# Optimization experiments

Measured on AMD Instinct MI355X. Metric: run time of the kernel, lower is better.

Reference implementation:

```python
import jax, jax.numpy as jnp
import numpy as np

T, B, X, Y = 24, 16, 64, 64
S, M, C = 16, 8, 8
F = S + M + C   # GRU input_size = 32
H = 32          # hidden_size


def setup_inputs() -> dict:
    key = jax.random.key(0)
    ks = jax.random.split(key, 8)
    inv = 1.0 / np.sqrt(H)
    return {
        "spatial": jax.random.normal(ks[0], (T, B, X, Y, S), dtype=jnp.float32),
        "meteorology": jax.random.normal(ks[1], (T, B, X, Y, M), dtype=jnp.float32),
        "context": jax.random.normal(ks[2], (T, B, X, Y, C), dtype=jnp.float32),
        # GRU parameters (torch layout: [3H, F] and [3H, H], gate order r,z,n)
        "W_ih": jax.random.uniform(ks[3], (3 * H, F), jnp.float32, -inv, inv),
        "W_hh": jax.random.uniform(ks[4], (3 * H, H), jnp.float32, -inv, inv),
        "b_ih": jax.random.uniform(ks[5], (3 * H,), jnp.float32, -inv, inv),
        "b_hh": jax.random.uniform(ks[6], (3 * H,), jnp.float32, -inv, inv),
        # output projection (hidden -> spatial_size)
        "W": jax.random.normal(ks[7], (H, S), dtype=jnp.float32),
    }


def reference(spatial, meteorology, context, W_ih, W_hh, b_ih, b_hh, W):
    # cat features: (T, B, X, Y, F); merge all pixels + batch into one GRU batch
    x = jnp.concatenate((spatial, meteorology, context), axis=4)
    N = B * X * Y
    x = x.reshape(T, N, F)

    # precompute input projections for all timesteps: (T, N, 3H)
    gx_all = jnp.einsum('tnf,gf->tng', x, W_ih) + b_ih

    def step(h, gx):
        gh = h @ W_hh.T + b_hh                      # (N, 3H)
        r = jax.nn.sigmoid(gx[:, :H] + gh[:, :H])
        z = jax.nn.sigmoid(gx[:, H:2 * H] + gh[:, H:2 * H])
        n = jnp.tanh(gx[:, 2 * H:] + r * gh[:, 2 * H:])
        h = (1.0 - z) * n + z * h
        return h, None

    h0 = jnp.zeros((N, H), dtype=x.dtype)
    h_final, _ = jax.lax.scan(step, h0, gx_all)     # (N, H)

    out = h_final @ W                               # (N, S)
    return out.reshape(B, X, Y, S)
```

## Files before the change

### kernel.cpp

```cpp
#include <hip/hip_runtime.h>
#include <hip/hip_bf16.h>


#define TSTEPS 24
#define NPIX 65536
#define PADW 40

typedef __attribute__((ext_vector_type(8))) short bf16x8;
typedef __attribute__((ext_vector_type(4))) float f32x4;
typedef __attribute__((ext_vector_type(4))) unsigned int u32x4;

#define MFMA16(a, b, c) __builtin_amdgcn_mfma_f32_16x16x32_bf16((a), (b), (c), 0, 0, 0)

#define SCL_RZ (-1.4426950408889634f)
#define SCL_N  ( 2.8853900817779268f)

__device__ __forceinline__ unsigned short f2bf(float f) {
  unsigned u = __builtin_bit_cast(unsigned, f);
  u += 0x7fffu + ((u >> 16) & 1u);
  return (unsigned short)(u >> 16);
}

__device__ __forceinline__ unsigned pk2(float a, float b) {
  __hip_bfloat162 h = __float22bfloat162_rn(float2{a, b});
  unsigned u;
  __builtin_memcpy(&u, &h, sizeof(u));
  return u;
}

__device__ __forceinline__ bf16x8 pack8(f32x4 a, f32x4 b) {
  u32x4 r = { pk2(a[0], a[1]), pk2(a[2], a[3]), pk2(b[0], b[1]), pk2(b[2], b[3]) };
  return __builtin_bit_cast(bf16x8, r);
}

__device__ __forceinline__ float sig2(float t) {
  return __builtin_amdgcn_rcpf(1.f + __builtin_amdgcn_exp2f(t));
}
__device__ __forceinline__ float tanh2(float t) {
  return 1.f - 2.f * __builtin_amdgcn_rcpf(1.f + __builtin_amdgcn_exp2f(t));
}

__device__ __forceinline__ bf16x8 relayout_h(const f32x4 h0, const f32x4 h1, int lane) {
  unsigned p00 = pk2(h0[0], h0[1]), p01 = pk2(h0[2], h0[3]);
  unsigned p10 = pk2(h1[0], h1[1]), p11 = pk2(h1[2], h1[3]);
  const int lo = (lane & 15) | ((lane & 16) << 1);
  const int hi = lo + 16;
  unsigned a0 = (unsigned)__shfl((int)p00, lo, 64);
  unsigned a1 = (unsigned)__shfl((int)p01, lo, 64);
  unsigned a2 = (unsigned)__shfl((int)p00, hi, 64);
  unsigned a3 = (unsigned)__shfl((int)p01, hi, 64);
  unsigned b0 = (unsigned)__shfl((int)p10, lo, 64);
  unsigned b1 = (unsigned)__shfl((int)p11, lo, 64);
  unsigned b2 = (unsigned)__shfl((int)p10, hi, 64);
  unsigned b3 = (unsigned)__shfl((int)p11, hi, 64);
  const bool t1 = (lane & 32) != 0;
  u32x4 d = { t1 ? b0 : a0, t1 ? b1 : a1, t1 ? b2 : a2, t1 ? b3 : a3 };
  return __builtin_bit_cast(bf16x8, d);
}

__global__ __launch_bounds__(256, 3)
void gru_fused(const float* __restrict__ spatial, const float* __restrict__ met,
               const float* __restrict__ ctx,
               const float* __restrict__ W_ih, const float* __restrict__ W_hh,
               const float* __restrict__ b_ih, const float* __restrict__ b_hh,
               const float* __restrict__ Wout, float* __restrict__ out) {
  __shared__ __align__(16) unsigned short sW[192 * PADW];
  __shared__ __align__(16) float sCB[64];
  __shared__ __align__(16) float sBIN[32];
  __shared__ __align__(16) float sBHN[32];

  const int tid = threadIdx.x;
  for (int i = tid; i < 96 * 32; i += 256) {
    int r = i >> 5, c = i & 31;
    float s = (r < 64) ? SCL_RZ : SCL_N;
    sW[r * PADW + c] = f2bf(W_ih[i] * s);
    sW[(96 + r) * PADW + c] = f2bf(W_hh[i] * s);
  }
  if (tid < 64) sCB[tid] = (b_ih[tid] + b_hh[tid]) * SCL_RZ;
  else if (tid < 96) sBIN[tid - 64] = b_ih[tid] * SCL_N;
  else if (tid < 128) sBHN[tid - 96] = b_hh[tid - 32] * SCL_N;
  __syncthreads();

  const int lane = tid & 63;
  const int col = lane & 15;
  const int q = lane >> 4;
  const int wave = blockIdx.x * 4 + (tid >> 6);
  const long p0 = (long)wave * 16 + col;

  f32x4 cS[4];
#pragma unroll
  for (int i = 0; i < 4; ++i) cS[i] = *(const f32x4*)&sCB[i * 16 + q * 4];
  const f32x4 cG4 = *(const f32x4*)&sBIN[q * 4];
  const f32x4 cG5 = *(const f32x4*)&sBIN[16 + q * 4];
  const f32x4 cH4 = *(const f32x4*)&sBHN[q * 4];
  const f32x4 cH5 = *(const f32x4*)&sBHN[16 + q * 4];

  const int wb = col * PADW + q * 8;
  const bf16x8 a0 = *(const bf16x8*)&sW[wb];
  const bf16x8 a1 = *(const bf16x8*)&sW[wb + 16 * PADW];
  const bf16x8 a2 = *(const bf16x8*)&sW[wb + 32 * PADW];
  const bf16x8 a3 = *(const bf16x8*)&sW[wb + 48 * PADW];
  const bf16x8 a4 = *(const bf16x8*)&sW[wb + 64 * PADW];
  const bf16x8 a5 = *(const bf16x8*)&sW[wb + 80 * PADW];
  const bf16x8 w0 = *(const bf16x8*)&sW[wb + 96 * PADW];
  const bf16x8 w1 = *(const bf16x8*)&sW[wb + 112 * PADW];
  const bf16x8 w2 = *(const bf16x8*)&sW[wb + 128 * PADW];
  const bf16x8 w3 = *(const bf16x8*)&sW[wb + 144 * PADW];
  const bf16x8 w4 = *(const bf16x8*)&sW[wb + 160 * PADW];
  const bf16x8 w5 = *(const bf16x8*)&sW[wb + 176 * PADW];

  const float* xp0;
  long xstride;
  if (q < 2) {
    xp0 = spatial + p0 * 16 + q * 8;
    xstride = (long)NPIX * 16;
  } else if (q == 2) {
    xp0 = met + p0 * 8; xstride = (long)NPIX * 8;
  } else {
    xp0 = ctx + p0 * 8; xstride = (long)NPIX * 8;
  }

  bf16x8 bx = pack8(*(const f32x4*)xp0, *(const f32x4*)(xp0 + 4));
  xp0 += xstride;

  f32x4 h0a = {0.f, 0.f, 0.f, 0.f}, h0b = {0.f, 0.f, 0.f, 0.f};
  const f32x4 zero = {0.f, 0.f, 0.f, 0.f};

#pragma unroll 1
  for (int t = 0; t < TSTEPS; ++t) {
    f32x4 xna, xnb;
    if (t < TSTEPS - 1) {
      xna = *(const f32x4*)xp0; xnb = *(const f32x4*)(xp0 + 4);
      xp0 += xstride;
    }

    f32x4 g0 = MFMA16(a0, bx, cS[0]);
    f32x4 g1 = MFMA16(a1, bx, cS[1]);
    f32x4 g2 = MFMA16(a2, bx, cS[2]);
    f32x4 g3 = MFMA16(a3, bx, cS[3]);
    f32x4 g4 = MFMA16(a4, bx, cG4);
    f32x4 g5 = MFMA16(a5, bx, cG5);

    bf16x8 bh = relayout_h(h0a, h0b, lane);

    f32x4 r0 = MFMA16(w0, bh, g0);
    f32x4 r1 = MFMA16(w1, bh, g1);
    f32x4 z0 = MFMA16(w2, bh, g2);
    f32x4 z1 = MFMA16(w3, bh, g3);
    f32x4 h4 = MFMA16(w4, bh, cH4);
    f32x4 h5 = MFMA16(w5, bh, cH5);

#pragma unroll
    for (int r = 0; r < 4; ++r) {
      float ra = sig2(r0[r]);
      float rb = sig2(r1[r]);
      float za = sig2(z0[r]);
      float zb = sig2(z1[r]);
      float na = tanh2(__builtin_fmaf(ra, h4[r], g4[r]));
      float nb = tanh2(__builtin_fmaf(rb, h5[r], g5[r]));
      h0a[r] = na + za * (h0a[r] - na);
      h0b[r] = nb + zb * (h0b[r] - nb);
    }

    if (t < TSTEPS - 1) bx = pack8(xna, xnb);
  }

  bf16x8 bhf = relayout_h(h0a, h0b, lane);
  float w[8];
#pragma unroll
  for (int j = 0; j < 8; ++j) w[j] = Wout[(q * 8 + j) * 16 + col];
  u32x4 awp = { pk2(w[0], w[1]), pk2(w[2], w[3]), pk2(w[4], w[5]), pk2(w[6], w[7]) };
  bf16x8 aw = __builtin_bit_cast(bf16x8, awp);
  f32x4 o0 = MFMA16(aw, bhf, zero);
  *(f32x4*)&out[p0 * 16 + q * 4] = o0;
}

extern "C" void kernel_launch(void* const* d_in, const int* in_sizes, int n_in,
                              void* d_out, int out_size, void* d_ws, size_t ws_size,
                              hipStream_t stream) {
  const float* spatial = (const float*)d_in[0];
  const float* met     = (const float*)d_in[1];
  const float* ctx     = (const float*)d_in[2];
  const float* W_ih    = (const float*)d_in[3];
  const float* W_hh    = (const float*)d_in[4];
  const float* b_ih    = (const float*)d_in[5];
  const float* b_hh    = (const float*)d_in[6];
  const float* Wout    = (const float*)d_in[7];
  float* out = (float*)d_out;

  gru_fused<<<dim3(NPIX / 16 / 4), dim3(256), 0, stream>>>(
      spatial, met, ctx, W_ih, W_hh, b_ih, b_hh, Wout, out);
}
```

Before: 240.8 us.

## Permute W_hh columns to drop hidden-state shuffles and process two pixel tiles per wave

W_hh columns (and the output projection rows) are permuted when loaded so the MFMA accumulator layout of h can be packed straight into the B operand, with no cross-lane shuffles. Each wave now handles two independent 16-pixel tiles, interleaving their MFMA chains and gate math to hide latency. The grid is halved and the launch-bounds occupancy hint drops from 3 to 2 blocks to make room for the extra registers. Fewer resident waves may reduce latency hiding elsewhere.

```diff
diff --git a/kernel.cpp b/kernel.cpp
--- a/kernel.cpp
+++ b/kernel.cpp
@@ -40,25 +40,12 @@
   return 1.f - 2.f * __builtin_amdgcn_rcpf(1.f + __builtin_amdgcn_exp2f(t));
 }
 
-__device__ __forceinline__ bf16x8 relayout_h(const f32x4 h0, const f32x4 h1, int lane) {
-  unsigned p00 = pk2(h0[0], h0[1]), p01 = pk2(h0[2], h0[3]);
-  unsigned p10 = pk2(h1[0], h1[1]), p11 = pk2(h1[2], h1[3]);
-  const int lo = (lane & 15) | ((lane & 16) << 1);
-  const int hi = lo + 16;
-  unsigned a0 = (unsigned)__shfl((int)p00, lo, 64);
-  unsigned a1 = (unsigned)__shfl((int)p01, lo, 64);
-  unsigned a2 = (unsigned)__shfl((int)p00, hi, 64);
-  unsigned a3 = (unsigned)__shfl((int)p01, hi, 64);
-  unsigned b0 = (unsigned)__shfl((int)p10, lo, 64);
-  unsigned b1 = (unsigned)__shfl((int)p11, lo, 64);
-  unsigned b2 = (unsigned)__shfl((int)p10, hi, 64);
-  unsigned b3 = (unsigned)__shfl((int)p11, hi, 64);
-  const bool t1 = (lane & 32) != 0;
-  u32x4 d = { t1 ? b0 : a0, t1 ? b1 : a1, t1 ? b2 : a2, t1 ? b3 : a3 };
-  return __builtin_bit_cast(bf16x8, d);
-}
-
-__global__ __launch_bounds__(256, 3)
+__device__ __forceinline__ int tau(int k) {
+  int q = k >> 3, j = k & 7;
+  return (j < 4) ? (q * 4 + j) : (16 + q * 4 + (j - 4));
+}
+
+__global__ __launch_bounds__(256, 2)
 void gru_fused(const float* __restrict__ spatial, const float* __restrict__ met,
                const float* __restrict__ ctx,
                const float* __restrict__ W_ih, const float* __restrict__ W_hh,
@@ -74,7 +61,7 @@
     int r = i >> 5, c = i & 31;
     float s = (r < 64) ? SCL_RZ : SCL_N;
     sW[r * PADW + c] = f2bf(W_ih[i] * s);
-    sW[(96 + r) * PADW + c] = f2bf(W_hh[i] * s);
+    sW[(96 + r) * PADW + c] = f2bf(W_hh[r * 32 + tau(c)] * s);
   }
   if (tid < 64) sCB[tid] = (b_ih[tid] + b_hh[tid]) * SCL_RZ;
   else if (tid < 96) sBIN[tid - 64] = b_ih[tid] * SCL_N;
@@ -85,7 +72,8 @@
   const int col = lane & 15;
   const int q = lane >> 4;
   const int wave = blockIdx.x * 4 + (tid >> 6);
-  const long p0 = (long)wave * 16 + col;
+  const long p0 = (long)wave * 32 + col;
+  const long p1 = p0 + 16;
 
   f32x4 cS[4];
 #pragma unroll
@@ -109,70 +97,92 @@
   const bf16x8 w4 = *(const bf16x8*)&sW[wb + 160 * PADW];
   const bf16x8 w5 = *(const bf16x8*)&sW[wb + 176 * PADW];
 
-  const float* xp0;
+  const float *xp0, *xp1;
   long xstride;
   if (q < 2) {
-    xp0 = spatial + p0 * 16 + q * 8;
+    xp0 = spatial + p0 * 16 + q * 8; xp1 = spatial + p1 * 16 + q * 8;
     xstride = (long)NPIX * 16;
   } else if (q == 2) {
-    xp0 = met + p0 * 8; xstride = (long)NPIX * 8;
+    xp0 = met + p0 * 8; xp1 = met + p1 * 8; xstride = (long)NPIX * 8;
   } else {
-    xp0 = ctx + p0 * 8; xstride = (long)NPIX * 8;
-  }
-
-  bf16x8 bx = pack8(*(const f32x4*)xp0, *(const f32x4*)(xp0 + 4));
-  xp0 += xstride;
+    xp0 = ctx + p0 * 8; xp1 = ctx + p1 * 8; xstride = (long)NPIX * 8;
+  }
+
+  bf16x8 bx0 = pack8(*(const f32x4*)xp0, *(const f32x4*)(xp0 + 4));
+  bf16x8 bx1 = pack8(*(const f32x4*)xp1, *(const f32x4*)(xp1 + 4));
+  xp0 += xstride; xp1 += xstride;
 
   f32x4 h0a = {0.f, 0.f, 0.f, 0.f}, h0b = {0.f, 0.f, 0.f, 0.f};
+  f32x4 h1a = {0.f, 0.f, 0.f, 0.f}, h1b = {0.f, 0.f, 0.f, 0.f};
   const f32x4 zero = {0.f, 0.f, 0.f, 0.f};
 
 #pragma unroll 1
   for (int t = 0; t < TSTEPS; ++t) {
-    f32x4 xna, xnb;
+    f32x4 xn0a, xn0b, xn1a, xn1b;
     if (t < TSTEPS - 1) {
-      xna = *(const f32x4*)xp0; xnb = *(const f32x4*)(xp0 + 4);
-      xp0 += xstride;
+      xn0a = *(const f32x4*)xp0; xn0b = *(const f32x4*)(xp0 + 4);
+      xn1a = *(const f32x4*)xp1; xn1b = *(const f32x4*)(xp1 + 4);
+      xp0 += xstride; xp1 += xstride;
     }
 
-    f32x4 g0 = MFMA16(a0, bx, cS[0]);
-    f32x4 g1 = MFMA16(a1, bx, cS[1]);
-    f32x4 g2 = MFMA16(a2, bx, cS[2]);
-    f32x4 g3 = MFMA16(a3, bx, cS[3]);
-    f32x4 g4 = MFMA16(a4, bx, cG4);
-    f32x4 g5 = MFMA16(a5, bx, cG5);
-
-    bf16x8 bh = relayout_h(h0a, h0b, lane);
-
-    f32x4 r0 = MFMA16(w0, bh, g0);
-    f32x4 r1 = MFMA16(w1, bh, g1);
-    f32x4 z0 = MFMA16(w2, bh, g2);
-    f32x4 z1 = MFMA16(w3, bh, g3);
-    f32x4 h4 = MFMA16(w4, bh, cH4);
-    f32x4 h5 = MFMA16(w5, bh, cH5);
+    bf16x8 bh0 = pack8(h0a, h0b);
+    bf16x8 bh1 = pack8(h1a, h1b);
+
+    f32x4 G00 = MFMA16(a0, bx0, cS[0]);  f32x4 G10 = MFMA16(a0, bx1, cS[0]);
+    f32x4 G01 = MFMA16(a1, bx0, cS[1]);  f32x4 G11 = MFMA16(a1, bx1, cS[1]);
+    f32x4 G02 = MFMA16(a2, bx0, cS[2]);  f32x4 G12 = MFMA16(a2, bx1, cS[2]);
+    f32x4 G03 = MFMA16(a3, bx0, cS[3]);  f32x4 G13 = MFMA16(a3, bx1, cS[3]);
+    f32x4 G04 = MFMA16(a4, bx0, cG4);    f32x4 G14 = MFMA16(a4, bx1, cG4);
+    f32x4 G05 = MFMA16(a5, bx0, cG5);    f32x4 G15 = MFMA16(a5, bx1, cG5);
+
+    f32x4 R00 = MFMA16(w0, bh0, G00);    f32x4 R10 = MFMA16(w0, bh1, G10);
+    f32x4 R01 = MFMA16(w1, bh0, G01);    f32x4 R11 = MFMA16(w1, bh1, G11);
+    f32x4 Z00 = MFMA16(w2, bh0, G02);    f32x4 Z10 = MFMA16(w2, bh1, G12);
+    f32x4 Z01 = MFMA16(w3, bh0, G03);    f32x4 Z11 = MFMA16(w3, bh1, G13);
+    f32x4 H04 = MFMA16(w4, bh0, cH4);    f32x4 H14 = MFMA16(w4, bh1, cH4);
+    f32x4 H05 = MFMA16(w5, bh0, cH5);    f32x4 H15 = MFMA16(w5, bh1, cH5);
 
 #pragma unroll
     for (int r = 0; r < 4; ++r) {
-      float ra = sig2(r0[r]);
-      float rb = sig2(r1[r]);
-      float za = sig2(z0[r]);
-      float zb = sig2(z1[r]);
-      float na = tanh2(__builtin_fmaf(ra, h4[r], g4[r]));
-      float nb = tanh2(__builtin_fmaf(rb, h5[r], g5[r]));
-      h0a[r] = na + za * (h0a[r] - na);
-      h0b[r] = nb + zb * (h0b[r] - nb);
+      float r00 = sig2(R00[r]);
+      float r01 = sig2(R01[r]);
+      float z00 = sig2(Z00[r]);
+      float z01 = sig2(Z01[r]);
+      float n00 = tanh2(__builtin_fmaf(r00, H04[r], G04[r]));
+      float n01 = tanh2(__builtin_fmaf(r01, H05[r], G05[r]));
+      h0a[r] = n00 + z00 * (h0a[r] - n00);
+      h0b[r] = n01 + z01 * (h0b[r] - n01);
+
+      float r10 = sig2(R10[r]);
+      float r11 = sig2(R11[r]);
+      float z10 = sig2(Z10[r]);
+      float z11 = sig2(Z11[r]);
+      float n10 = tanh2(__builtin_fmaf(r10, H14[r], G14[r]));
+      float n11 = tanh2(__builtin_fmaf(r11, H15[r], G15[r]));
+      h1a[r] = n10 + z10 * (h1a[r] - n10);
+      h1b[r] = n11 + z11 * (h1b[r] - n11);
     }
 
-    if (t < TSTEPS - 1) bx = pack8(xna, xnb);
-  }
-
-  bf16x8 bhf = relayout_h(h0a, h0b, lane);
+    if (t < TSTEPS - 1) {
+      bx0 = pack8(xn0a, xn0b);
+      bx1 = pack8(xn1a, xn1b);
+    }
+  }
+
+  bf16x8 bhf0 = pack8(h0a, h0b);
+  bf16x8 bhf1 = pack8(h1a, h1b);
   float w[8];
 #pragma unroll
-  for (int j = 0; j < 8; ++j) w[j] = Wout[(q * 8 + j) * 16 + col];
+  for (int j = 0; j < 8; ++j) {
+    int tk = (j < 4) ? (q * 4 + j) : (16 + q * 4 + (j - 4));
+    w[j] = Wout[tk * 16 + col];
+  }
   u32x4 awp = { pk2(w[0], w[1]), pk2(w[2], w[3]), pk2(w[4], w[5]), pk2(w[6], w[7]) };
   bf16x8 aw = __builtin_bit_cast(bf16x8, awp);
-  f32x4 o0 = MFMA16(aw, bhf, zero);
+  f32x4 o0 = MFMA16(aw, bhf0, zero);
+  f32x4 o1 = MFMA16(aw, bhf1, zero);
   *(f32x4*)&out[p0 * 16 + q * 4] = o0;
+  *(f32x4*)&out[p1 * 16 + q * 4] = o1;
 }
 
 extern "C" void kernel_launch(void* const* d_in, const int* in_sizes, int n_in,
@@ -188,6 +198,6 @@
   const float* Wout    = (const float*)d_in[7];
   float* out = (float*)d_out;
 
-  gru_fused<<<dim3(NPIX / 16 / 4), dim3(256), 0, stream>>>(
+  gru_fused<<<dim3(NPIX / 32 / 4), dim3(256), 0, stream>>>(
       spatial, met, ctx, W_ih, W_hh, b_ih, b_hh, Wout, out);
 }
```

Measured after the change: 230.3 us. 1.05x faster.
